# Kernel optimization log

Hardware: AMD Instinct MI355X
Metric: run time of the kernel (lower is better)

## Reference

```python
import jax, jax.numpy as jnp
import numpy as np
import math

B, S, H, Dh, Dr, HID, C = 2, 2048, 16, 128, 64, 2048, 512

def _linear(x, w, b):
    return x @ w.T + b

def _rope(x):
    # x: [B, H, S, Dr]; interleaved-pair rotation as in the torch module
    d = x.shape[-1]
    s = x.shape[2]
    inv_freq = 1.0 / (10000.0 ** (jnp.arange(0, d, 2, dtype=jnp.float32) / d))
    sinusoid = jnp.arange(s, dtype=jnp.float32)[:, None] * inv_freq[None, :]  # [S, d/2]
    sin, cos = jnp.sin(sinusoid), jnp.cos(sinusoid)  # broadcast over B,H
    x1 = x[..., 0::2]
    x2 = x[..., 1::2]
    rot = jnp.stack([x1 * cos - x2 * sin, x1 * sin + x2 * cos], axis=-1)
    return rot.reshape(x.shape)

def setup_inputs() -> dict:
    key = jax.random.key(0)
    ks = jax.random.split(key, 9)
    sc = 0.02
    return {
        "x": jax.random.normal(ks[0], (B, S, HID), jnp.float32),
        "d_kv_w": jax.random.normal(ks[1], (C, HID), jnp.float32) * sc,
        "d_kv_b": jnp.zeros((C,), jnp.float32),
        "u_k_w": jax.random.normal(ks[2], (H * Dh, C), jnp.float32) * sc,
        "u_k_b": jnp.zeros((H * Dh,), jnp.float32),
        "u_v_w": jax.random.normal(ks[3], (H * Dh, C), jnp.float32) * sc,
        "u_v_b": jnp.zeros((H * Dh,), jnp.float32),
        "d_q_w": jax.random.normal(ks[4], (C, HID), jnp.float32) * sc,
        "d_q_b": jnp.zeros((C,), jnp.float32),
        "u_q_w": jax.random.normal(ks[5], (H * Dh, C), jnp.float32) * sc,
        "u_q_b": jnp.zeros((H * Dh,), jnp.float32),
        "qr_w": jax.random.normal(ks[6], (H * Dr, C), jnp.float32) * sc,
        "qr_b": jnp.zeros((H * Dr,), jnp.float32),
        "out_w": jax.random.normal(ks[7], (HID, H * Dh), jnp.float32) * sc,
        "out_b": jnp.zeros((HID,), jnp.float32),
    }

def reference(x, d_kv_w, d_kv_b, u_k_w, u_k_b, u_v_w, u_v_b,
              d_q_w, d_q_b, u_q_w, u_q_b, qr_w, qr_b, out_w, out_b):
    b, s, _ = x.shape
    kv_c = _linear(x, d_kv_w, d_kv_b)                      # [B,S,C]
    k_c = _linear(kv_c, u_k_w, u_k_b).reshape(b, s, H, Dh)
    k_r = _linear(kv_c, qr_w, qr_b).reshape(b, s, H, Dr)   # note: qr_proj reused, as in source
    v = _linear(kv_c, u_v_w, u_v_b).reshape(b, s, H, Dh)
    q_c_lat = _linear(x, d_q_w, d_q_b)                     # [B,S,C]
    q_c = _linear(q_c_lat, u_q_w, u_q_b).reshape(b, s, H, Dh)
    q_r = _linear(q_c_lat, qr_w, qr_b).reshape(b, s, H, Dr)
    # RoPE operates on [B,H,S,Dr]
    q_r = _rope(q_r.transpose(0, 2, 1, 3)).transpose(0, 2, 1, 3)
    k_r = _rope(k_r.transpose(0, 2, 1, 3)).transpose(0, 2, 1, 3)
    q = jnp.concatenate([q_c, q_r], axis=-1)               # [B,S,H,Dh+Dr]
    k = jnp.concatenate([k_c, k_r], axis=-1)
    scale = 1.0 / math.sqrt(Dh + Dr)
    scores = jnp.einsum('bqhd,bkhd->bhqk', q, k) * scale   # [B,H,S,S]
    probs = jax.nn.softmax(scores, axis=-1)
    ctx = jnp.einsum('bhqk,bkhd->bqhd', probs, v).reshape(b, s, H * Dh)
    return _linear(ctx, out_w, out_b)
```

## Files before the change

kernel.cpp:

```cpp
#include <hip/hip_runtime.h>
#include <hip/hip_bf16.h>
#include <math.h>
#include <stdint.h>

#define NB 2
#define NS 2048
#define NH 16
#define NDH 128
#define NDR 64
#define NHID 2048
#define NC 512

typedef unsigned short u16;
typedef short short8 __attribute__((ext_vector_type(8)));
typedef short short4v __attribute__((ext_vector_type(4)));
typedef float f32x4 __attribute__((ext_vector_type(4)));

__device__ __forceinline__ u16 f2bf(float f) {
  union { float f; uint32_t u; } c; c.f = f;
  uint32_t u = c.u + 0x7fffu + ((c.u >> 16) & 1u);
  return (u16)(u >> 16);
}
__device__ __forceinline__ float bf2f(u16 b) {
  union { uint32_t u; float f; } c; c.u = ((uint32_t)b) << 16;
  return c.f;
}
__device__ __forceinline__ void async16(const void* g, void* l) {
  __builtin_amdgcn_global_load_lds((const __attribute__((address_space(1))) void*)g,
                                   (__attribute__((address_space(3))) void*)l, 16, 0, 0);
}
__device__ __forceinline__ uint32_t cvtpk(float a, float b) {
  uint32_t r;
  asm("v_cvt_pk_bf16_f32 %0, %1, %2" : "=v"(r) : "v"(a), "v"(b));
  return r;
}

struct CastArgs {
  const float* src[8];
  u16* dst[8];
  int start[8];
};

__global__ __launch_bounds__(256) void cast_kernel(CastArgs a) {
  int blk = blockIdx.x;
  int ti = 0;
#pragma unroll
  for (int i = 1; i < 8; ++i) ti += (blk >= a.start[i]) ? 1 : 0;
  size_t off = (size_t)(blk - a.start[ti]) * 2048 + (size_t)threadIdx.x * 8;
  const float4* s = (const float4*)(a.src[ti] + off);
  float4 v0 = s[0], v1 = s[1];
  u16 o[8];
  o[0] = f2bf(v0.x); o[1] = f2bf(v0.y); o[2] = f2bf(v0.z); o[3] = f2bf(v0.w);
  o[4] = f2bf(v1.x); o[5] = f2bf(v1.y); o[6] = f2bf(v1.z); o[7] = f2bf(v1.w);
  *(short8*)(a.dst[ti] + off) = *(short8*)o;
}

struct GemmSeg {
  const u16* A;
  const u16* W;
  const float* bias;
  void* dst;
  int K;
  int mode;
  int ldc;
};
struct GemmArgs {
  GemmSeg seg[5];
  int nbstart[6];
  int nseg;
};

__global__ __launch_bounds__(256) void gemm_bt(GemmArgs ga) {
  __shared__ u16 la[128 * 32];
  __shared__ u16 lb[128 * 32];
  const int nb = blockIdx.x, mb = blockIdx.y;
  int si = 0;
  for (int i = 1; i < ga.nseg; ++i) si += (nb >= ga.nbstart[i]) ? 1 : 0;
  GemmSeg sg = ga.seg[si];
  const int nbl = nb - ga.nbstart[si];
  const int K = sg.K;
  const u16* Ap = sg.A + (size_t)mb * 128 * K;
  const u16* Wp = sg.W + (size_t)nbl * 128 * K;
  const int t = threadIdx.x;
  const int l = t & 63, w = t >> 6;
  const int r0 = t >> 2, c0 = (t & 3) * 8;
  const int wm = (w >> 1) * 64, wn = (w & 1) * 64;
  const int frow = l & 15, fk = (l >> 4) * 8;
  const u16* laf = &la[(wm + frow) * 32 + fk];
  const u16* lbf = &lb[(wn + frow) * 32 + fk];

  const f32x4 vzero = {0.f, 0.f, 0.f, 0.f};
  f32x4 acc[4][4];
#pragma unroll
  for (int i = 0; i < 4; ++i)
#pragma unroll
    for (int j = 0; j < 4; ++j) acc[i][j] = vzero;

  for (int kt = 0; kt < K; kt += 32) {
    async16(Ap + (size_t)r0 * K + kt + c0, ((char*)la) + t * 16);
    async16(Ap + (size_t)(r0 + 64) * K + kt + c0, ((char*)la) + 4096 + t * 16);
    async16(Wp + (size_t)r0 * K + kt + c0, ((char*)lb) + t * 16);
    async16(Wp + (size_t)(r0 + 64) * K + kt + c0, ((char*)lb) + 4096 + t * 16);
    __syncthreads();
    short8 af[4], bfr[4];
#pragma unroll
    for (int i = 0; i < 4; ++i) af[i] = *(const short8*)(laf + i * 512);
#pragma unroll
    for (int j = 0; j < 4; ++j) bfr[j] = *(const short8*)(lbf + j * 512);
#pragma unroll
    for (int i = 0; i < 4; ++i)
#pragma unroll
      for (int j = 0; j < 4; ++j)
        acc[i][j] = __builtin_amdgcn_mfma_f32_16x16x32_bf16(af[i], bfr[j], acc[i][j], 0, 0, 0);
    __syncthreads();
  }

  const int rb = (l >> 4) * 4;
  const int cl = l & 15;
  if (sg.mode == 0) {
    u16* D = (u16*)sg.dst;
#pragma unroll
    for (int i = 0; i < 4; ++i)
#pragma unroll
      for (int j = 0; j < 4; ++j) {
        int col = nbl * 128 + wn + j * 16 + cl;
        float bv = sg.bias[col];
#pragma unroll
        for (int r = 0; r < 4; ++r) {
          int row = mb * 128 + wm + i * 16 + rb + r;
          D[(size_t)row * sg.ldc + col] = f2bf(acc[i][j][r] + bv);
        }
      }
  } else if (sg.mode == 2) {
    float* D = (float*)sg.dst;
#pragma unroll
    for (int i = 0; i < 4; ++i)
#pragma unroll
      for (int j = 0; j < 4; ++j) {
        int col = nbl * 128 + wn + j * 16 + cl;
        float bv = sg.bias[col];
#pragma unroll
        for (int r = 0; r < 4; ++r) {
          int row = mb * 128 + wm + i * 16 + rb + r;
          D[(size_t)row * sg.ldc + col] = acc[i][j][r] + bv;
        }
      }
  } else {
    u16* D = (u16*)sg.dst;
#pragma unroll
    for (int i = 0; i < 4; ++i) {
      int row0 = mb * 128 + wm + i * 16 + rb;
      int bb = row0 >> 11, ss = row0 & (NS - 1);
#pragma unroll
      for (int j = 0; j < 4; ++j) {
        int col = nbl * 128 + wn + j * 16 + cl;
        int hh = col >> 7, dv = col & 127;
        float bv = sg.bias[col];
        u16 pk[4];
#pragma unroll
        for (int r = 0; r < 4; ++r) pk[r] = f2bf(acc[i][j][r] + bv);
        *(short4v*)(D + ((size_t)((bb * NH + hh) * NDH + dv)) * NS + ss) = *(short4v*)pk;
      }
    }
  }
}

__global__ __launch_bounds__(256) void rope_kernel(u16* kr, u16* qr) {
  int tid = blockIdx.x * 256 + threadIdx.x;
  int which = tid >> 19;
  int loc = tid & ((1 << 19) - 1);
  int row = loc >> 7;
  int ch = loc & 127;
  int s = row & (NS - 1);
  u16* p = (which ? qr : kr) + (size_t)row * (NH * NDR) + ch * 8;
  short8 v = *(short8*)p;
  int jb = (ch & 7) * 4;
  u16 o[8];
#pragma unroll
  for (int q = 0; q < 4; ++q) {
    int j = jb + q;
    float invf = exp2f(-(float)j * 0.41524101186f);
    float ang = (float)s * invf;
    float sn = sinf(ang), cs = cosf(ang);
    float x1 = bf2f(((u16*)&v)[2 * q]);
    float x2 = bf2f(((u16*)&v)[2 * q + 1]);
    o[2 * q]     = f2bf(x1 * cs - x2 * sn);
    o[2 * q + 1] = f2bf(x1 * sn + x2 * cs);
  }
  *(short8*)p = *(short8*)o;
}

__global__ __launch_bounds__(256, 2) void attn_kernel(
    const u16* __restrict__ Qc, const u16* __restrict__ Qr,
    const u16* __restrict__ Kc, const u16* __restrict__ Kr,
    const u16* __restrict__ VT, u16* __restrict__ Ctx) {
  extern __shared__ char smem[];
  const int t = threadIdx.x, w = t >> 6, l = t & 63;
  const int g = l >> 4, cl = l & 15;
  const int lin = blockIdx.x;
  const int xcd = lin & 7, idx = lin >> 3;
  const int bh = xcd * 4 + (idx >> 4);
  const int qb = idx & 15;
  const int b = bh >> 4, h = bh & 15;
  const int q0 = qb * 128 + w * 32;

  short8 qf[2][6];
#pragma unroll
  for (int qr = 0; qr < 2; ++qr) {
    const u16* qc = Qc + ((size_t)(b * NS + q0 + qr * 16 + cl)) * NHID + h * NDH + g * 8;
    const u16* qrp = Qr + ((size_t)(b * NS + q0 + qr * 16 + cl)) * (NH * NDR) + h * NDR + g * 8;
#pragma unroll
    for (int c = 0; c < 4; ++c) qf[qr][c] = *(const short8*)(qc + c * 32);
    qf[qr][4] = *(const short8*)(qrp);
    qf[qr][5] = *(const short8*)(qrp + 32);
  }
#pragma unroll
  for (int qr = 0; qr < 2; ++qr)
#pragma unroll
    for (int c = 0; c < 6; ++c) asm volatile("" :: "v"(qf[qr][c]));

  const u16* kptr[6]; int kstep[6];
#pragma unroll
  for (int r = 0; r < 6; ++r) {
    int Lb = r * 4096 + t * 16;
    int row = Lb / 384;
    int off = Lb - row * 384;
    int c = (off ^ ((row & 7) << 4)) >> 1;
    if (c < NDH) { kptr[r] = Kc + ((size_t)(b * NS + row)) * NHID + h * NDH + c; kstep[r] = 64 * NHID; }
    else { kptr[r] = Kr + ((size_t)(b * NS + row)) * (NH * NDR) + h * NDR + (c - NDH); kstep[r] = 64 * NH * NDR; }
  }
  const u16* vptr[4];
#pragma unroll
  for (int r = 0; r < 4; ++r) {
    int Lb = r * 4096 + t * 16;
    int row = Lb >> 7, off = Lb & 127;
    int c = (off ^ ((row & 7) << 4)) >> 1;
    vptr[r] = VT + ((size_t)(bh * NDH + row)) * NS + c;
  }

  float m2[2] = {-1e30f, -1e30f};
  float lsum[2] = {0.f, 0.f};
  const f32x4 vzero = {0.f, 0.f, 0.f, 0.f};
  f32x4 o[2][8];
#pragma unroll
  for (int qr = 0; qr < 2; ++qr)
#pragma unroll
    for (int d = 0; d < 8; ++d) o[qr][d] = vzero;
  const float scale2 = 0.10411757f;

  {
    char* base = smem;
#pragma unroll
    for (int r = 0; r < 6; ++r) { async16(kptr[r], base + r * 4096 + t * 16); kptr[r] += kstep[r]; }
#pragma unroll
    for (int r = 0; r < 4; ++r) { async16(vptr[r], base + 24576 + r * 4096 + t * 16); vptr[r] += 64; }
  }

  for (int kv = 0; kv < NS / 64; ++kv) {
    const char* cur = smem + (size_t)(kv & 1) * 40960;
    if (kv < NS / 64 - 1) {
      char* nxt = smem + (size_t)((kv + 1) & 1) * 40960;
#pragma unroll
      for (int r = 0; r < 6; ++r) { async16(kptr[r], nxt + r * 4096 + t * 16); kptr[r] += kstep[r]; }
#pragma unroll
      for (int r = 0; r < 4; ++r) { async16(vptr[r], nxt + 24576 + r * 4096 + t * 16); vptr[r] += 64; }
      asm volatile("s_waitcnt vmcnt(10)" ::: "memory");
    } else {
      asm volatile("s_waitcnt vmcnt(0)" ::: "memory");
    }
    __builtin_amdgcn_s_barrier();
    asm volatile("" ::: "memory");

    const u16* kt = (const u16*)cur;
    const u16* vt = (const u16*)(cur + 24576);

    f32x4 sa[2][4];
#pragma unroll
    for (int qr = 0; qr < 2; ++qr)
#pragma unroll
      for (int n = 0; n < 4; ++n) sa[qr][n] = vzero;
#pragma unroll
    for (int n = 0; n < 4; ++n) {
      int krow = n * 16 + cl;
      const char* kb = ((const char*)kt) + krow * 384;
      int xo = (krow & 7) << 4;
      short8 kf[6];
#pragma unroll
      for (int c = 0; c < 6; ++c) kf[c] = *(const short8*)(kb + ((c * 64 + g * 16) ^ xo));
      __builtin_amdgcn_s_setprio(1);
#pragma unroll
      for (int c = 0; c < 6; ++c) {
        sa[0][n] = __builtin_amdgcn_mfma_f32_16x16x32_bf16(kf[c], qf[0][c], sa[0][n], 0, 0, 0);
        sa[1][n] = __builtin_amdgcn_mfma_f32_16x16x32_bf16(kf[c], qf[1][c], sa[1][n], 0, 0, 0);
      }
      __builtin_amdgcn_s_setprio(0);
    }

    short4v pb[2][4];
#pragma unroll
    for (int qr = 0; qr < 2; ++qr) {
      float mx = fmaxf(fmaxf(sa[qr][0][0], sa[qr][0][1]), fmaxf(sa[qr][0][2], sa[qr][0][3]));
#pragma unroll
      for (int n = 1; n < 4; ++n)
        mx = fmaxf(mx, fmaxf(fmaxf(sa[qr][n][0], sa[qr][n][1]), fmaxf(sa[qr][n][2], sa[qr][n][3])));
      mx = fmaxf(mx, __shfl_xor(mx, 16));
      mx = fmaxf(mx, __shfl_xor(mx, 32));
      float mxs = mx * scale2;
      if (!__all(mxs <= m2[qr] + 6.0f)) {
        float mn = fmaxf(m2[qr], mxs);
        float sf = exp2f(m2[qr] - mn);
        m2[qr] = mn;
        lsum[qr] *= sf;
        f32x4 sfv = {sf, sf, sf, sf};
#pragma unroll
        for (int d = 0; d < 8; ++d) o[qr][d] *= sfv;
      }
      float nm = -m2[qr];
      float ps = 0.f;
#pragma unroll
      for (int n = 0; n < 4; ++n) {
        float p0 = exp2f(fmaf(sa[qr][n][0], scale2, nm));
        float p1 = exp2f(fmaf(sa[qr][n][1], scale2, nm));
        float p2 = exp2f(fmaf(sa[qr][n][2], scale2, nm));
        float p3 = exp2f(fmaf(sa[qr][n][3], scale2, nm));
        ps += (p0 + p1) + (p2 + p3);
        union { uint32_t u[2]; short4v s; } pu;
        pu.u[0] = cvtpk(p0, p1);
        pu.u[1] = cvtpk(p2, p3);
        pb[qr][n] = pu.s;
      }
      ps += __shfl_xor(ps, 16);
      ps += __shfl_xor(ps, 32);
      lsum[qr] += ps;
    }

#pragma unroll
    for (int n = 0; n < 4; ++n) {
      __builtin_amdgcn_s_setprio(1);
#pragma unroll
      for (int d = 0; d < 8; ++d) {
        int vrow = d * 16 + cl;
        const char* vb = ((const char*)vt) + vrow * 128;
        short4v va = *(const short4v*)(vb + ((n * 32 + g * 8) ^ ((vrow & 7) << 4)));
        o[0][d] = __builtin_amdgcn_mfma_f32_16x16x16bf16_1k(va, pb[0][n], o[0][d], 0, 0, 0);
        o[1][d] = __builtin_amdgcn_mfma_f32_16x16x16bf16_1k(va, pb[1][n], o[1][d], 0, 0, 0);
      }
      __builtin_amdgcn_s_setprio(0);
    }

    asm volatile("s_waitcnt lgkmcnt(0)" ::: "memory");
    __builtin_amdgcn_s_barrier();
  }

#pragma unroll
  for (int qr = 0; qr < 2; ++qr) {
    float invq = 1.f / lsum[qr];
    u16* dst = Ctx + ((size_t)(b * NS + q0 + qr * 16 + cl)) * NHID + h * NDH + g * 4;
#pragma unroll
    for (int d = 0; d < 8; ++d) {
      float a0 = o[qr][d][0] * invq, a1 = o[qr][d][1] * invq;
      float a2 = o[qr][d][2] * invq, a3 = o[qr][d][3] * invq;
      union { uint32_t u[2]; short4v s; } pu;
      pu.u[0] = cvtpk(a0, a1);
      pu.u[1] = cvtpk(a2, a3);
      *(short4v*)(dst + d * 16) = pu.s;
    }
  }
}

extern "C" void kernel_launch(void* const* d_in, const int* in_sizes, int n_in,
                              void* d_out, int out_size, void* d_ws, size_t ws_size,
                              hipStream_t stream) {
  (void)in_sizes; (void)n_in; (void)out_size;
  const float* x      = (const float*)d_in[0];
  const float* d_kv_w = (const float*)d_in[1];
  const float* d_kv_b = (const float*)d_in[2];
  const float* u_k_w  = (const float*)d_in[3];
  const float* u_k_b  = (const float*)d_in[4];
  const float* u_v_w  = (const float*)d_in[5];
  const float* u_v_b  = (const float*)d_in[6];
  const float* d_q_w  = (const float*)d_in[7];
  const float* d_q_b  = (const float*)d_in[8];
  const float* u_q_w  = (const float*)d_in[9];
  const float* u_q_b  = (const float*)d_in[10];
  const float* qr_w   = (const float*)d_in[11];
  const float* qr_b   = (const float*)d_in[12];
  const float* out_w  = (const float*)d_in[13];
  const float* out_b  = (const float*)d_in[14];

  char* ws = (char*)d_ws;
  size_t off = 0;
  auto alloc = [&](size_t bytes) -> void* {
    void* p = ws + off;
    off += (bytes + 255) & ~(size_t)255;
    return p;
  };
  u16* xb   = (u16*)alloc((size_t)NB * NS * NHID * 2);
  u16* wdkv = (u16*)alloc((size_t)NC * NHID * 2);
  u16* wuk  = (u16*)alloc((size_t)NH * NDH * NC * 2);
  u16* wuv  = (u16*)alloc((size_t)NH * NDH * NC * 2);
  u16* wdq  = (u16*)alloc((size_t)NC * NHID * 2);
  u16* wuq  = (u16*)alloc((size_t)NH * NDH * NC * 2);
  u16* wqr  = (u16*)alloc((size_t)NH * NDR * NC * 2);
  u16* wout = (u16*)alloc((size_t)NHID * NH * NDH * 2);
  u16* kvc  = (u16*)alloc((size_t)NB * NS * NC * 2);
  u16* qlat = (u16*)alloc((size_t)NB * NS * NC * 2);
  u16* Kc   = (u16*)alloc((size_t)NB * NS * NH * NDH * 2);
  u16* Krt  = (u16*)alloc((size_t)NB * NS * NH * NDR * 2);
  u16* Qc   = (u16*)alloc((size_t)NB * NS * NH * NDH * 2);
  u16* Qrt  = (u16*)alloc((size_t)NB * NS * NH * NDR * 2);
  u16* VT   = (u16*)alloc((size_t)NB * NH * NDH * NS * 2);
  u16* ctx  = xb;
  if (off > ws_size) return;

  {
    CastArgs ca;
    const float* srcs[8] = {x, d_kv_w, u_k_w, u_v_w, d_q_w, u_q_w, qr_w, out_w};
    u16* dsts[8] = {xb, wdkv, wuk, wuv, wdq, wuq, wqr, wout};
    int sizes[8] = {NB * NS * NHID, NC * NHID, NH * NDH * NC, NH * NDH * NC,
                    NC * NHID, NH * NDH * NC, NH * NDR * NC, NHID * NH * NDH};
    int st = 0;
    for (int i = 0; i < 8; ++i) {
      ca.src[i] = srcs[i]; ca.dst[i] = dsts[i]; ca.start[i] = st;
      st += sizes[i] / 2048;
    }
    cast_kernel<<<dim3(st), dim3(256), 0, stream>>>(ca);
  }

  {
    GemmArgs ga;
    ga.nseg = 2;
    ga.seg[0] = {xb, wdkv, d_kv_b, kvc, NHID, 0, NC};
    ga.seg[1] = {xb, wdq,  d_q_b,  qlat, NHID, 0, NC};
    for (int i = 2; i < 5; ++i) ga.seg[i] = ga.seg[0];
    ga.nbstart[0] = 0; ga.nbstart[1] = 4; ga.nbstart[2] = 8;
    ga.nbstart[3] = 8; ga.nbstart[4] = 8; ga.nbstart[5] = 8;
    gemm_bt<<<dim3(8, 32), dim3(256), 0, stream>>>(ga);
  }

  {
    GemmArgs ga;
    ga.nseg = 5;
    ga.seg[0] = {kvc,  wuk, u_k_b, Kc,  NC, 0, NH * NDH};
    ga.seg[1] = {kvc,  wuv, u_v_b, VT,  NC, 1, 0};
    ga.seg[2] = {kvc,  wqr, qr_b,  Krt, NC, 0, NH * NDR};
    ga.seg[3] = {qlat, wuq, u_q_b, Qc,  NC, 0, NH * NDH};
    ga.seg[4] = {qlat, wqr, qr_b,  Qrt, NC, 0, NH * NDR};
    ga.nbstart[0] = 0;  ga.nbstart[1] = 16; ga.nbstart[2] = 32;
    ga.nbstart[3] = 40; ga.nbstart[4] = 56; ga.nbstart[5] = 64;
    gemm_bt<<<dim3(64, 32), dim3(256), 0, stream>>>(ga);
  }

  rope_kernel<<<dim3(4096), dim3(256), 0, stream>>>(Krt, Qrt);

  hipFuncSetAttribute((const void*)attn_kernel,
                      hipFuncAttributeMaxDynamicSharedMemorySize, 81920);
  attn_kernel<<<dim3(512), dim3(256), 81920, stream>>>(Qc, Qrt, Kc, Krt, VT, ctx);

  {
    GemmArgs ga;
    ga.nseg = 1;
    ga.seg[0] = {ctx, wout, out_b, d_out, NHID, 2, NHID};
    for (int i = 1; i < 5; ++i) ga.seg[i] = ga.seg[0];
    ga.nbstart[0] = 0;
    for (int i = 1; i < 6; ++i) ga.nbstart[i] = 16;
    gemm_bt<<<dim3(16, 32), dim3(256), 0, stream>>>(ga);
  }
}
```

Baseline: 313.4 us.

## Double-buffer GEMM LDS loads and unroll attention loop with constant buffer offsets

The projection GEMM moves from a single LDS buffer with two __syncthreads per k-tile to a double-buffered async pipeline. The next tile's global-to-LDS loads are issued before the current tile is computed, and the code waits on a partial vmcnt. The attention loop is unrolled by two with compile-time buffer offsets, and swizzled K/V LDS addresses are precomputed once, which cuts per-iteration address arithmetic. The cost is double the GEMM LDS footprint (32KB), which may lower occupancy, and more code size.

```diff
diff --git a/kernel.cpp b/kernel.cpp
--- a/kernel.cpp
+++ b/kernel.cpp
@@ -15,6 +15,8 @@
 typedef short short8 __attribute__((ext_vector_type(8)));
 typedef short short4v __attribute__((ext_vector_type(4)));
 typedef float f32x4 __attribute__((ext_vector_type(4)));
+
+template <int V> struct IC { static constexpr int value = V; };
 
 __device__ __forceinline__ u16 f2bf(float f) {
   union { float f; uint32_t u; } c; c.f = f;
@@ -71,23 +73,31 @@
 };
 
 __global__ __launch_bounds__(256) void gemm_bt(GemmArgs ga) {
-  __shared__ u16 la[128 * 32];
-  __shared__ u16 lb[128 * 32];
+  __shared__ char glds[32768];
   const int nb = blockIdx.x, mb = blockIdx.y;
   int si = 0;
   for (int i = 1; i < ga.nseg; ++i) si += (nb >= ga.nbstart[i]) ? 1 : 0;
   GemmSeg sg = ga.seg[si];
   const int nbl = nb - ga.nbstart[si];
   const int K = sg.K;
-  const u16* Ap = sg.A + (size_t)mb * 128 * K;
-  const u16* Wp = sg.W + (size_t)nbl * 128 * K;
   const int t = threadIdx.x;
   const int l = t & 63, w = t >> 6;
   const int r0 = t >> 2, c0 = (t & 3) * 8;
   const int wm = (w >> 1) * 64, wn = (w & 1) * 64;
   const int frow = l & 15, fk = (l >> 4) * 8;
-  const u16* laf = &la[(wm + frow) * 32 + fk];
-  const u16* lbf = &lb[(wn + frow) * 32 + fk];
+  const int lafO = ((wm + frow) * 32 + fk) * 2;
+  const int lbfO = 8192 + ((wn + frow) * 32 + fk) * 2;
+
+  const u16* apA = sg.A + (size_t)mb * 128 * K + (size_t)r0 * K + c0;
+  const u16* wpA = sg.W + (size_t)nbl * 128 * K + (size_t)r0 * K + c0;
+
+  auto stage = [&](int bufOff) {
+    async16(apA, glds + bufOff + t * 16);
+    async16(apA + (size_t)64 * K, glds + bufOff + 4096 + t * 16);
+    async16(wpA, glds + bufOff + 8192 + t * 16);
+    async16(wpA + (size_t)64 * K, glds + bufOff + 12288 + t * 16);
+    apA += 32; wpA += 32;
+  };
 
   const f32x4 vzero = {0.f, 0.f, 0.f, 0.f};
   f32x4 acc[4][4];
@@ -96,23 +106,38 @@
 #pragma unroll
     for (int j = 0; j < 4; ++j) acc[i][j] = vzero;
 
-  for (int kt = 0; kt < K; kt += 32) {
-    async16(Ap + (size_t)r0 * K + kt + c0, ((char*)la) + t * 16);
-    async16(Ap + (size_t)(r0 + 64) * K + kt + c0, ((char*)la) + 4096 + t * 16);
-    async16(Wp + (size_t)r0 * K + kt + c0, ((char*)lb) + t * 16);
-    async16(Wp + (size_t)(r0 + 64) * K + kt + c0, ((char*)lb) + 4096 + t * 16);
-    __syncthreads();
+  stage(0);
+  const int nk = K / 32;
+
+  auto ktile = [&](auto bufc, bool stageNext) {
+    constexpr int BO = decltype(bufc)::value;
+    if (stageNext) {
+      stage(BO ^ 16384);
+      asm volatile("s_waitcnt vmcnt(4)" ::: "memory");
+    } else {
+      asm volatile("s_waitcnt vmcnt(0)" ::: "memory");
+    }
+    __builtin_amdgcn_s_barrier();
+    asm volatile("" ::: "memory");
     short8 af[4], bfr[4];
 #pragma unroll
-    for (int i = 0; i < 4; ++i) af[i] = *(const short8*)(laf + i * 512);
-#pragma unroll
-    for (int j = 0; j < 4; ++j) bfr[j] = *(const short8*)(lbf + j * 512);
+    for (int i = 0; i < 4; ++i) af[i] = *(const short8*)(glds + BO + lafO + i * 1024);
+#pragma unroll
+    for (int j = 0; j < 4; ++j) bfr[j] = *(const short8*)(glds + BO + lbfO + j * 1024);
+    __builtin_amdgcn_s_setprio(1);
 #pragma unroll
     for (int i = 0; i < 4; ++i)
 #pragma unroll
       for (int j = 0; j < 4; ++j)
         acc[i][j] = __builtin_amdgcn_mfma_f32_16x16x32_bf16(af[i], bfr[j], acc[i][j], 0, 0, 0);
-    __syncthreads();
+    __builtin_amdgcn_s_setprio(0);
+    asm volatile("s_waitcnt lgkmcnt(0)" ::: "memory");
+    __builtin_amdgcn_s_barrier();
+  };
+
+  for (int kk = 0; kk < nk; kk += 2) {
+    ktile(IC<0>{}, true);
+    ktile(IC<16384>{}, kk + 2 < nk);
   }
 
   const int rb = (l >> 4) * 4;
@@ -238,6 +263,13 @@
     vptr[r] = VT + ((size_t)(bh * NDH + row)) * NS + c;
   }
 
+  const int xo = (cl & 7) << 4;
+  int kaddr[6], vaddr[4];
+#pragma unroll
+  for (int c = 0; c < 6; ++c) kaddr[c] = cl * 384 + ((c * 64 + g * 16) ^ xo);
+#pragma unroll
+  for (int n = 0; n < 4; ++n) vaddr[n] = 24576 + cl * 128 + ((n * 32 + g * 8) ^ xo);
+
   float m2[2] = {-1e30f, -1e30f};
   float lsum[2] = {0.f, 0.f};
   const f32x4 vzero = {0.f, 0.f, 0.f, 0.f};
@@ -248,22 +280,18 @@
     for (int d = 0; d < 8; ++d) o[qr][d] = vzero;
   const float scale2 = 0.10411757f;
 
-  {
-    char* base = smem;
-#pragma unroll
-    for (int r = 0; r < 6; ++r) { async16(kptr[r], base + r * 4096 + t * 16); kptr[r] += kstep[r]; }
-#pragma unroll
-    for (int r = 0; r < 4; ++r) { async16(vptr[r], base + 24576 + r * 4096 + t * 16); vptr[r] += 64; }
-  }
-
-  for (int kv = 0; kv < NS / 64; ++kv) {
-    const char* cur = smem + (size_t)(kv & 1) * 40960;
-    if (kv < NS / 64 - 1) {
-      char* nxt = smem + (size_t)((kv + 1) & 1) * 40960;
-#pragma unroll
-      for (int r = 0; r < 6; ++r) { async16(kptr[r], nxt + r * 4096 + t * 16); kptr[r] += kstep[r]; }
-#pragma unroll
-      for (int r = 0; r < 4; ++r) { async16(vptr[r], nxt + 24576 + r * 4096 + t * 16); vptr[r] += 64; }
+  auto stage_into = [&](int bufOff) {
+#pragma unroll
+    for (int r = 0; r < 6; ++r) { async16(kptr[r], smem + bufOff + r * 4096 + t * 16); kptr[r] += kstep[r]; }
+#pragma unroll
+    for (int r = 0; r < 4; ++r) { async16(vptr[r], smem + bufOff + 24576 + r * 4096 + t * 16); vptr[r] += 64; }
+  };
+  stage_into(0);
+
+  auto tile = [&](auto bufc, bool stageNext) {
+    constexpr int BO = decltype(bufc)::value;
+    if (stageNext) {
+      stage_into(BO ^ 40960);
       asm volatile("s_waitcnt vmcnt(10)" ::: "memory");
     } else {
       asm volatile("s_waitcnt vmcnt(0)" ::: "memory");
@@ -271,9 +299,6 @@
     __builtin_amdgcn_s_barrier();
     asm volatile("" ::: "memory");
 
-    const u16* kt = (const u16*)cur;
-    const u16* vt = (const u16*)(cur + 24576);
-
     f32x4 sa[2][4];
 #pragma unroll
     for (int qr = 0; qr < 2; ++qr)
@@ -281,12 +306,10 @@
       for (int n = 0; n < 4; ++n) sa[qr][n] = vzero;
 #pragma unroll
     for (int n = 0; n < 4; ++n) {
-      int krow = n * 16 + cl;
-      const char* kb = ((const char*)kt) + krow * 384;
-      int xo = (krow & 7) << 4;
       short8 kf[6];
 #pragma unroll
-      for (int c = 0; c < 6; ++c) kf[c] = *(const short8*)(kb + ((c * 64 + g * 16) ^ xo));
+      for (int c = 0; c < 6; ++c)
+        kf[c] = *(const short8*)(smem + kaddr[c] + (BO + n * 6144));
       __builtin_amdgcn_s_setprio(1);
 #pragma unroll
       for (int c = 0; c < 6; ++c) {
@@ -339,9 +362,7 @@
       __builtin_amdgcn_s_setprio(1);
 #pragma unroll
       for (int d = 0; d < 8; ++d) {
-        int vrow = d * 16 + cl;
-        const char* vb = ((const char*)vt) + vrow * 128;
-        short4v va = *(const short4v*)(vb + ((n * 32 + g * 8) ^ ((vrow & 7) << 4)));
+        short4v va = *(const short4v*)(smem + vaddr[n] + (BO + d * 2048));
         o[0][d] = __builtin_amdgcn_mfma_f32_16x16x16bf16_1k(va, pb[0][n], o[0][d], 0, 0, 0);
         o[1][d] = __builtin_amdgcn_mfma_f32_16x16x16bf16_1k(va, pb[1][n], o[1][d], 0, 0, 0);
       }
@@ -350,6 +371,11 @@
 
     asm volatile("s_waitcnt lgkmcnt(0)" ::: "memory");
     __builtin_amdgcn_s_barrier();
+  };
+
+  for (int kv = 0; kv < NS / 64; kv += 2) {
+    tile(IC<0>{}, true);
+    tile(IC<40960>{}, kv + 2 < NS / 64);
   }
 
 #pragma unroll
```

Result: faster. 303.7 us (-3.1%).
